# Kernel tuning notes

Measured on AMD Instinct MI355X. Metric: run time of the kernel, lower is better.

The kernel has to match this reference:

```python
import jax, jax.numpy as jnp
import numpy as np

N_NODES = 100000
N_EDGES = 3200000
EMBED_DIM = 64


def setup_inputs() -> dict:
    key = jax.random.key(0)
    k1, k2, k3, k4 = jax.random.split(key, 4)
    x = jax.random.normal(k1, (N_NODES, EMBED_DIM), dtype=jnp.float32)
    adj_rows = jax.random.randint(k2, (N_EDGES,), 0, N_NODES, dtype=jnp.int64)
    adj_cols = jax.random.randint(k3, (N_EDGES,), 0, N_NODES, dtype=jnp.int64)
    adj_vals = jax.random.uniform(k4, (N_EDGES,), dtype=jnp.float32)
    return {"x": x, "adj_rows": adj_rows, "adj_cols": adj_cols, "adj_vals": adj_vals}


def reference(x, adj_rows, adj_cols, adj_vals):
    # out = adj @ x, adj sparse COO: out[r] += v * x[c] for each (r, c, v)
    messages = x[adj_cols] * adj_vals[:, None]          # [E, D]
    out = jax.ops.segment_sum(messages, adj_rows, num_segments=N_NODES)  # [N, D]
    return out
```

## Files before the change

### kernel.cpp

```cpp
#include <hip/hip_runtime.h>
#include <hip/hip_fp16.h>

#define EMBED_DIM 64
#define NBMAX 1024
#define RPB 128
#define RPB_SHIFT 7
#define CAP 6144
#define CHUNK 8192
#define SCAT_T 512
#define EPT (CHUNK / SCAT_T)
#define SENTINEL_KEY 0xFFFFFFFFu

typedef float f32x8 __attribute__((ext_vector_type(8)));
typedef float f32x4 __attribute__((ext_vector_type(4)));

__device__ __forceinline__ int load_idx(const void* p, int e, bool i64) {
    return i64 ? (int)((const long long*)p)[e] : ((const int*)p)[e];
}

__device__ __forceinline__ float h2f(ushort u) {
    __half_raw hr; hr.x = u;
    return __half2float(__half(hr));
}

static inline size_t align_up(size_t v, size_t a) { return (v + a - 1) & ~(a - 1); }

__global__ __launch_bounds__(1024) void detect_zero_kernel(
    const unsigned int* __restrict__ rows_u32, int* __restrict__ flag,
    int* __restrict__ gcur, int nb) {
    const int tid = threadIdx.x;
    if (tid == 0) {
        int nz = 0;
        for (int i = 1; i < 128; i += 2) nz += (rows_u32[i] != 0u);
        *flag = (nz == 0) ? 1 : 0;
    }
    if (tid < nb) gcur[tid] = 0;
}

__global__ __launch_bounds__(256) void xconv_kernel(
    const float* __restrict__ x, ushort* __restrict__ xh, int n8) {
    int i = blockIdx.x * 256 + threadIdx.x;
    if (i >= n8) return;
    float4 a = ((const float4*)x)[i * 2];
    float4 b = ((const float4*)x)[i * 2 + 1];
    ushort h[8];
    h[0] = __half_as_ushort(__float2half_rn(a.x));
    h[1] = __half_as_ushort(__float2half_rn(a.y));
    h[2] = __half_as_ushort(__float2half_rn(a.z));
    h[3] = __half_as_ushort(__float2half_rn(a.w));
    h[4] = __half_as_ushort(__float2half_rn(b.x));
    h[5] = __half_as_ushort(__float2half_rn(b.y));
    h[6] = __half_as_ushort(__float2half_rn(b.z));
    h[7] = __half_as_ushort(__float2half_rn(b.w));
    ((uint4*)xh)[i] = *(const uint4*)h;
}

__global__ __launch_bounds__(SCAT_T) void bscatter_kernel(
    const void* __restrict__ rows_p, const void* __restrict__ cols_p,
    const float* __restrict__ vals, int* __restrict__ gcur,
    uint2* __restrict__ recs, const int* __restrict__ flag_p, int n_edges) {
    __shared__ int h[NBMAX];
    __shared__ int base[NBMAX];
    const bool i64 = (*flag_p != 0);
    const int tid = threadIdx.x;
    const int c0 = blockIdx.x * CHUNK;
    int rloc[EPT];

    for (int i = tid; i < NBMAX; i += SCAT_T) h[i] = 0;
    __syncthreads();

    #pragma unroll
    for (int k = 0; k < EPT; ++k) {
        int e = c0 + k * SCAT_T + tid;
        int r = (e < n_edges) ? load_idx(rows_p, e, i64) : -1;
        rloc[k] = r;
        if (r >= 0) atomicAdd(&h[r >> RPB_SHIFT], 1);
    }
    __syncthreads();

    for (int i = tid; i < NBMAX; i += SCAT_T) {
        int c = h[i];
        int ca = (c + 7) & ~7;
        base[i] = c ? (i * CAP + atomicAdd(&gcur[i], ca)) : 0;
        h[i] = 0;
    }
    __syncthreads();

    #pragma unroll
    for (int k0 = 0; k0 < EPT; k0 += 4) {
        int cc[4]; float vv[4];
        #pragma unroll
        for (int j = 0; j < 4; ++j) {
            int e = c0 + (k0 + j) * SCAT_T + tid;
            if (rloc[k0 + j] >= 0) {
                cc[j] = load_idx(cols_p, e, i64);
                vv[j] = vals[e];
            }
        }
        #pragma unroll
        for (int j = 0; j < 4; ++j) {
            int r = rloc[k0 + j];
            if (r >= 0) {
                int b = r >> RPB_SHIFT;
                int pos = base[b] + atomicAdd(&h[b], 1);
                if (pos < (b + 1) * CAP)
                    recs[pos] = make_uint2(
                        ((unsigned)(r & (RPB - 1)) << 20) | (unsigned)cc[j],
                        __float_as_uint(vv[j]));
            }
        }
    }
    __syncthreads();

    for (int i = tid; i < NBMAX; i += SCAT_T) {
        int c = h[i];
        if (c > 0) {
            int ca = (c + 7) & ~7;
            for (int j = c; j < ca; ++j) {
                int pos = base[i] + j;
                if (pos < (i + 1) * CAP)
                    recs[pos] = make_uint2(SENTINEL_KEY, 0u);
            }
        }
    }
}

__global__ __launch_bounds__(512) void bsort_kernel(
    const int* __restrict__ gcur, const uint2* __restrict__ recs,
    uint2* __restrict__ recs2, uint2* __restrict__ srange, int N) {
    __shared__ int cnt[RPB];
    __shared__ int scn[RPB];
    __shared__ int rbase[RPB];
    const int b = blockIdx.x;
    const int tid = threadIdx.x;
    const int s = b * CAP;
    int n = gcur[b];
    if (n > CAP) n = CAP;

    if (tid < RPB) cnt[tid] = 0;
    __syncthreads();

    for (int i = tid; i < n; i += 512) {
        unsigned lr = recs[s + i].x >> 20;
        if (lr < RPB) atomicAdd(&cnt[lr], 1);
    }
    __syncthreads();

    if (tid < RPB) scn[tid] = cnt[tid];
    __syncthreads();
    for (int d = 1; d < RPB; d <<= 1) {
        int u = (tid < RPB && tid >= d) ? scn[tid - d] : 0;
        __syncthreads();
        if (tid < RPB) scn[tid] += u;
        __syncthreads();
    }
    if (tid < RPB) {
        int excl = scn[tid] - cnt[tid];
        rbase[tid] = excl;
        int row = b * RPB + tid;
        if (row < N) srange[row] = make_uint2(s + excl, s + excl + cnt[tid]);
        cnt[tid] = 0;
    }
    __syncthreads();

    for (int i = tid; i < n; i += 512) {
        uint2 e = recs[s + i];
        unsigned lr = e.x >> 20;
        if (lr < RPB) {
            int pos = s + rbase[lr] + atomicAdd(&cnt[lr], 1);
            recs2[pos] = make_uint2(e.x & 0xFFFFFu, e.y);
        }
    }
}

__global__ __launch_bounds__(256) void gather_kernel(
    const uint2* __restrict__ srange, const uint2* __restrict__ recs2,
    const ushort* __restrict__ xh, float* __restrict__ out, int N) {
    int t = blockIdx.x * blockDim.x + threadIdx.x;
    int row = t >> 3;
    if (row >= N) return;
    const int lane = t & 7;

    uint2 rg = srange[row];
    int e = (int)rg.x;
    const int e_end = (int)rg.y;
    f32x8 A = {};

    #define ACC8(U, V)                                                     \
        {                                                                  \
            float2 f0 = __half22float2(*(const __half2*)&(U).x);           \
            float2 f1 = __half22float2(*(const __half2*)&(U).y);           \
            float2 f2 = __half22float2(*(const __half2*)&(U).z);           \
            float2 f3 = __half22float2(*(const __half2*)&(U).w);           \
            A[0] += (V) * f0.x; A[1] += (V) * f0.y;                        \
            A[2] += (V) * f1.x; A[3] += (V) * f1.y;                        \
            A[4] += (V) * f2.x; A[5] += (V) * f2.y;                        \
            A[6] += (V) * f3.x; A[7] += (V) * f3.y;                        \
        }

    for (; e + 4 <= e_end; e += 4) {
        uint2 r0 = recs2[e],     r1 = recs2[e + 1];
        uint2 r2 = recs2[e + 2], r3 = recs2[e + 3];
        uint4 a0 = ((const uint4*)(xh + (size_t)r0.x * EMBED_DIM))[lane];
        uint4 a1 = ((const uint4*)(xh + (size_t)r1.x * EMBED_DIM))[lane];
        uint4 a2 = ((const uint4*)(xh + (size_t)r2.x * EMBED_DIM))[lane];
        uint4 a3 = ((const uint4*)(xh + (size_t)r3.x * EMBED_DIM))[lane];
        float v0 = __uint_as_float(r0.y), v1 = __uint_as_float(r1.y);
        float v2 = __uint_as_float(r2.y), v3 = __uint_as_float(r3.y);
        ACC8(a0, v0); ACC8(a1, v1); ACC8(a2, v2); ACC8(a3, v3);
    }
    for (; e < e_end; ++e) {
        uint2 r0 = recs2[e];
        uint4 a0 = ((const uint4*)(xh + (size_t)r0.x * EMBED_DIM))[lane];
        ACC8(a0, __uint_as_float(r0.y));
    }
    #undef ACC8

    f32x4 o0 = {A[0], A[1], A[2], A[3]};
    f32x4 o1 = {A[4], A[5], A[6], A[7]};
    f32x4* op = (f32x4*)(out + (size_t)row * EMBED_DIM) + lane * 2;
    __builtin_nontemporal_store(o0, op);
    __builtin_nontemporal_store(o1, op + 1);
}

__global__ __launch_bounds__(256) void spmv_coo_kernel(
    const void* __restrict__ rows_p, const void* __restrict__ cols_p,
    const float* __restrict__ vals, const float* __restrict__ x,
    float* __restrict__ out, const int* __restrict__ flag_p, int n_edges) {
    const bool i64 = (*flag_p != 0);
    const int lane16 = threadIdx.x & 15;
    long long t      = (long long)blockIdx.x * blockDim.x + threadIdx.x;
    long long stride = (long long)gridDim.x * blockDim.x;
    long long total  = (long long)n_edges * 16;
    for (; t < total; t += stride) {
        int e = (int)(t >> 4);
        int r = load_idx(rows_p, e, i64);
        int c = load_idx(cols_p, e, i64);
        float v = vals[e];
        float4 xv = ((const float4*)(x + (long long)c * EMBED_DIM))[lane16];
        float* o = out + (long long)r * EMBED_DIM + lane16 * 4;
        unsafeAtomicAdd(o + 0, xv.x * v);
        unsafeAtomicAdd(o + 1, xv.y * v);
        unsafeAtomicAdd(o + 2, xv.z * v);
        unsafeAtomicAdd(o + 3, xv.w * v);
    }
}

extern "C" void kernel_launch(void* const* d_in, const int* in_sizes, int n_in,
                              void* d_out, int out_size, void* d_ws, size_t ws_size,
                              hipStream_t stream) {
    const float* x    = (const float*)d_in[0];
    const void*  rows = d_in[1];
    const void*  cols = d_in[2];
    const float* vals = (const float*)d_in[3];
    float* out = (float*)d_out;
    const int E = in_sizes[1];
    const int N = out_size / EMBED_DIM;
    const int NB = (N + RPB - 1) >> RPB_SHIFT;

    char* ws = (char*)d_ws;
    size_t off = 0;
    int* flag = (int*)(ws + off);            off += 16;
    int* gcur = (int*)(ws + off);            off += (size_t)NBMAX * 4;
    off = align_up(off, 256);
    ushort* xh = (ushort*)(ws + off);        off += (size_t)N * EMBED_DIM * 2;
    off = align_up(off, 256);
    uint2* srange = (uint2*)(ws + off);      off += (size_t)N * 8;
    off = align_up(off, 256);
    uint2* recs = (uint2*)(ws + off);        off += (size_t)NB * CAP * 8;
    off = align_up(off, 256);
    uint2* recs2 = (uint2*)(ws + off);       off += (size_t)NB * CAP * 8;
    const size_t needed = off;

    if (ws_size < needed || NB > NBMAX || N > (1 << 20) ||
        (size_t)NB * CAP < (size_t)E / 2) {
        detect_zero_kernel<<<1, 1024, 0, stream>>>((const unsigned int*)rows,
                                                   flag, gcur, 0);
        (void)hipMemsetAsync(d_out, 0, (size_t)out_size * sizeof(float), stream);
        spmv_coo_kernel<<<8192, 256, 0, stream>>>(rows, cols, vals, x, out,
                                                  flag, E);
        return;
    }

    detect_zero_kernel<<<1, 1024, 0, stream>>>((const unsigned int*)rows,
                                               flag, gcur, NB);
    xconv_kernel<<<(N * 8 + 255) / 256, 256, 0, stream>>>(x, xh, N * 8);
    const int grid_c = (E + CHUNK - 1) / CHUNK;
    bscatter_kernel<<<grid_c, SCAT_T, 0, stream>>>(rows, cols, vals, gcur,
                                                   recs, flag, E);
    bsort_kernel<<<NB, 512, 0, stream>>>(gcur, recs, recs2, srange, N);
    const int grid_g = (N * 8 + 255) / 256;
    gather_kernel<<<grid_g, 256, 0, stream>>>(srange, recs2, xh, out, N);
}
```

Baseline: 151.9 us.

## Stage scattered bucket records in LDS and write them out coalesced

The bucket scatter kernel now runs a block-wide prefix scan over per-bucket counts so each record can be placed into a local LDS staging buffer first. After staging, each wavefront copies whole bucket segments to global memory with contiguous lane writes, padding with sentinels. This replaces many scattered 8-byte global stores with coalesced runs. In exchange it adds a 512-step-class scan with many barriers and about 78 KB of dynamic LDS per block, which reduces how many blocks fit on a CU.

```diff
diff --git a/kernel.cpp b/kernel.cpp
--- a/kernel.cpp
+++ b/kernel.cpp
@@ -10,17 +10,13 @@
 #define SCAT_T 512
 #define EPT (CHUNK / SCAT_T)
 #define SENTINEL_KEY 0xFFFFFFFFu
+#define SCAT_LDS (NBMAX * 4 * 3 + 512 * 4 + CHUNK * 8)
 
 typedef float f32x8 __attribute__((ext_vector_type(8)));
 typedef float f32x4 __attribute__((ext_vector_type(4)));
 
 __device__ __forceinline__ int load_idx(const void* p, int e, bool i64) {
     return i64 ? (int)((const long long*)p)[e] : ((const int*)p)[e];
-}
-
-__device__ __forceinline__ float h2f(ushort u) {
-    __half_raw hr; hr.x = u;
-    return __half2float(__half(hr));
 }
 
 static inline size_t align_up(size_t v, size_t a) { return (v + a - 1) & ~(a - 1); }
@@ -58,12 +54,18 @@
 __global__ __launch_bounds__(SCAT_T) void bscatter_kernel(
     const void* __restrict__ rows_p, const void* __restrict__ cols_p,
     const float* __restrict__ vals, int* __restrict__ gcur,
-    uint2* __restrict__ recs, const int* __restrict__ flag_p, int n_edges) {
-    __shared__ int h[NBMAX];
-    __shared__ int base[NBMAX];
+    uint2* __restrict__ recs, const int* __restrict__ flag_p,
+    int n_edges, int nb) {
+    extern __shared__ char smem[];
+    int*   h     = (int*)smem;
+    int*   gbase = h + NBMAX;
+    int*   lbase = gbase + NBMAX;
+    int*   tsum  = lbase + NBMAX;
+    uint2* rec   = (uint2*)(tsum + 512);
+
     const bool i64 = (*flag_p != 0);
     const int tid = threadIdx.x;
-    const int c0 = blockIdx.x * CHUNK;
+    const int c0e = blockIdx.x * CHUNK;
     int rloc[EPT];
 
     for (int i = tid; i < NBMAX; i += SCAT_T) h[i] = 0;
@@ -71,18 +73,33 @@
 
     #pragma unroll
     for (int k = 0; k < EPT; ++k) {
-        int e = c0 + k * SCAT_T + tid;
+        int e = c0e + k * SCAT_T + tid;
         int r = (e < n_edges) ? load_idx(rows_p, e, i64) : -1;
         rloc[k] = r;
         if (r >= 0) atomicAdd(&h[r >> RPB_SHIFT], 1);
     }
     __syncthreads();
 
-    for (int i = tid; i < NBMAX; i += SCAT_T) {
-        int c = h[i];
-        int ca = (c + 7) & ~7;
-        base[i] = c ? (i * CAP + atomicAdd(&gcur[i], ca)) : 0;
-        h[i] = 0;
+    const int b0 = 2 * tid, b1 = 2 * tid + 1;
+    int cb0 = h[b0], cb1 = h[b1];
+    int s = cb0 + cb1;
+    tsum[tid] = s;
+    __syncthreads();
+    for (int d = 1; d < 512; d <<= 1) {
+        int u = (tid >= d) ? tsum[tid - d] : 0;
+        __syncthreads();
+        tsum[tid] += u;
+        __syncthreads();
+    }
+    {
+        int run = tsum[tid] - s;
+        lbase[b0] = run;
+        lbase[b1] = run + cb0;
+        int a0 = (cb0 + 7) & ~7, a1 = (cb1 + 7) & ~7;
+        gbase[b0] = cb0 ? (b0 * CAP + atomicAdd(&gcur[b0], a0)) : 0;
+        gbase[b1] = cb1 ? (b1 * CAP + atomicAdd(&gcur[b1], a1)) : 0;
+        h[b0] = 0;
+        h[b1] = 0;
     }
     __syncthreads();
 
@@ -91,7 +108,7 @@
         int cc[4]; float vv[4];
         #pragma unroll
         for (int j = 0; j < 4; ++j) {
-            int e = c0 + (k0 + j) * SCAT_T + tid;
+            int e = c0e + (k0 + j) * SCAT_T + tid;
             if (rloc[k0 + j] >= 0) {
                 cc[j] = load_idx(cols_p, e, i64);
                 vv[j] = vals[e];
@@ -102,25 +119,26 @@
             int r = rloc[k0 + j];
             if (r >= 0) {
                 int b = r >> RPB_SHIFT;
-                int pos = base[b] + atomicAdd(&h[b], 1);
-                if (pos < (b + 1) * CAP)
-                    recs[pos] = make_uint2(
-                        ((unsigned)(r & (RPB - 1)) << 20) | (unsigned)cc[j],
-                        __float_as_uint(vv[j]));
+                int pos = lbase[b] + atomicAdd(&h[b], 1);
+                rec[pos] = make_uint2(
+                    ((unsigned)(r & (RPB - 1)) << 20) | (unsigned)cc[j],
+                    __float_as_uint(vv[j]));
             }
         }
     }
     __syncthreads();
 
-    for (int i = tid; i < NBMAX; i += SCAT_T) {
-        int c = h[i];
-        if (c > 0) {
-            int ca = (c + 7) & ~7;
-            for (int j = c; j < ca; ++j) {
-                int pos = base[i] + j;
-                if (pos < (i + 1) * CAP)
-                    recs[pos] = make_uint2(SENTINEL_KEY, 0u);
-            }
+    const int wave = tid >> 6, lane = tid & 63;
+    for (int b = wave; b < nb; b += (SCAT_T / 64)) {
+        int c = h[b];
+        if (c == 0) continue;
+        int ca = (c + 7) & ~7;
+        int gb = gbase[b], lb = lbase[b];
+        int lim = (b + 1) * CAP;
+        for (int j = lane; j < ca; j += 64) {
+            uint2 v = (j < c) ? rec[lb + j] : make_uint2(SENTINEL_KEY, 0u);
+            int pos = gb + j;
+            if (pos < lim) recs[pos] = v;
         }
     }
 }
@@ -286,8 +304,8 @@
                                                flag, gcur, NB);
     xconv_kernel<<<(N * 8 + 255) / 256, 256, 0, stream>>>(x, xh, N * 8);
     const int grid_c = (E + CHUNK - 1) / CHUNK;
-    bscatter_kernel<<<grid_c, SCAT_T, 0, stream>>>(rows, cols, vals, gcur,
-                                                   recs, flag, E);
+    bscatter_kernel<<<grid_c, SCAT_T, SCAT_LDS, stream>>>(
+        rows, cols, vals, gcur, recs, flag, E, NB);
     bsort_kernel<<<NB, 512, 0, stream>>>(gcur, recs, recs2, srange, N);
     const int grid_g = (N * 8 + 255) / 256;
     gather_kernel<<<grid_g, 256, 0, stream>>>(srange, recs2, xh, out, N);
```

Result: slower. 159.9 us (+5.3%).
